# Performance work log

Hardware: AMD Instinct MI355X
Metric: run time of the kernel (lower is better)

Reference implementation:

```python
import jax, jax.numpy as jnp
import numpy as np

B, S, D, E, K = 4, 4096, 2048, 64, 8

def setup_inputs() -> dict:
    key = jax.random.key(0)
    k1, k2 = jax.random.split(key, 2)
    x = jax.random.normal(k1, (B, S, D), dtype=jnp.float32)
    # centroid projection params (Dense(features=n_experts))
    W = jax.random.normal(k2, (D, E), dtype=jnp.float32) / np.sqrt(D).astype(np.float32)
    b = jnp.zeros((E,), dtype=jnp.float32)
    return {"x": x, "W": W, "b": b, "k": K}

def reference(x, W, b, k):
    # dense gating projection + sigmoid -> per-token expert scores [B,S,E]
    scores = jax.nn.sigmoid(jnp.einsum('bsd,de->bse', x, W) + b)
    # per-token top-k expert selection (vectorized form of apply_along_axis(top))
    g_i, idx = jax.lax.top_k(scores, k)          # [B,S,k]
    g = g_i / jnp.sum(g_i, axis=-1, keepdims=True)  # renormalize top-k gates
    return g, idx, scores
```

## Files before the change

kernel.cpp:

```cpp
#include <hip/hip_runtime.h>
#include <math.h>
#include <stdint.h>

#define NTOK   16384
#define DDIM   2048
#define NE     64
#define TOPK   8

#define THREADS 512
#define TOKPB   16
#define BK      64
#define NCHUNK  (DDIM / BK)

#define XSLOTS   (TOKPB * (BK / 4))
#define WSLOTS   (BK * (NE / 4))
#define BUFSLOTS (XSLOTS + WSLOTS)
#define SMEMF4   (2 * BUFSLOTS)

__device__ __forceinline__ void gl_lds16(const void* g, void* l) {
    __builtin_amdgcn_global_load_lds(
        (const __attribute__((address_space(1))) void*)(uintptr_t)g,
        (__attribute__((address_space(3))) void*)(uintptr_t)l,
        16, 0, 0);
}

__global__ __launch_bounds__(THREADS, 6) void gate_kernel(
    const float* __restrict__ x, const float* __restrict__ W,
    const float* __restrict__ b, float* __restrict__ out)
{
    __shared__ float4 smem[SMEMF4];

    const int tid  = threadIdx.x;
    const int wave = tid >> 6;
    const int lane = tid & 63;
    const int ks   = tid >> 5;
    const int tg   = (tid >> 4) & 1;
    const int eg   = tid & 15;
    const int tok0 = blockIdx.x * TOKPB;

    const float* gx  = x + (size_t)(tok0 + wave * 4 + (lane >> 4)) * DDIM
                         + (lane & 15) * 4;
    const float* gw0 = W + (size_t)(wave * 8 + (lane >> 4)) * NE + (lane & 15) * 4;
    const float* gw1 = gw0 + (size_t)4 * NE;

    auto stage = [&](int c) {
        float4* Bf = &smem[(c & 1) * BUFSLOTS];
        const int kc = c * BK;
        if (wave < 4) gl_lds16(gx + kc, &Bf[wave * 64]);
        gl_lds16(gw0 + (size_t)kc * NE, &Bf[XSLOTS + wave * 128]);
        gl_lds16(gw1 + (size_t)kc * NE, &Bf[XSLOTS + wave * 128 + 64]);
    };

    float acc[8][4];
#pragma unroll
    for (int i = 0; i < 8; ++i)
#pragma unroll
        for (int m = 0; m < 4; ++m) acc[i][m] = 0.f;

    auto compute = [&](int c) {
        const float4* BX = &smem[(c & 1) * BUFSLOTS];
        const float4* BW = BX + XSLOTS;
        float4 wreg[4];
#pragma unroll
        for (int kk = 0; kk < 4; ++kk)
            wreg[kk] = BW[(ks * 4 + kk) * 16 + eg];
#pragma unroll
        for (int i = 0; i < 8; ++i) {
            const float4 xv = BX[(tg * 8 + i) * 16 + ks];
            const float* xp = (const float*)&xv;
#pragma unroll
            for (int kk = 0; kk < 4; ++kk) {
                const float xs = xp[kk];
                const float* wp = (const float*)&wreg[kk];
#pragma unroll
                for (int m = 0; m < 4; ++m)
                    acc[i][m] = fmaf(xs, wp[m], acc[i][m]);
            }
        }
    };

    stage(0);
#pragma unroll 1
    for (int c = 0; c < NCHUNK; ++c) {
        __syncthreads();
        if (c + 1 < NCHUNK) stage(c + 1);
        __builtin_amdgcn_s_setprio(1);
        compute(c);
        __builtin_amdgcn_s_setprio(0);
    }
    __syncthreads();

#pragma unroll
    for (int i = 0; i < 8; ++i)
#pragma unroll
        for (int m = 0; m < 4; ++m)
            acc[i][m] += __shfl_xor(acc[i][m], 32);

    float4* part4 = (float4*)smem;
    const int p = lane & 31;
    if (lane < 32) {
        float4* dst = part4 + (wave * 32 + p) * 9;
#pragma unroll
        for (int i = 0; i < 8; ++i)
            dst[i] = make_float4(acc[i][0], acc[i][1], acc[i][2], acc[i][3]);
    }
    __syncthreads();

    float* out_g   = out;
    float* out_idx = out + (size_t)NTOK * TOPK;
    float* out_s   = out + (size_t)NTOK * TOPK * 2;

    const int t  = tid >> 4;
    const int e4 = tid & 15;
    float4 sg = make_float4(0.f, 0.f, 0.f, 0.f);
    if (tid < 256) {
        const int cp = ((t >> 3) << 4) + e4;
        const int cf = t & 7;
        float sx = 0.f, sy = 0.f, sz = 0.f, sw = 0.f;
#pragma unroll
        for (int w = 0; w < 8; ++w) {
            const float4 v = part4[(w * 32 + cp) * 9 + cf];
            sx += v.x; sy += v.y; sz += v.z; sw += v.w;
        }
        const float4 bv = *(const float4*)(b + e4 * 4);
        sg.x = 1.f / (1.f + expf(-(sx + bv.x)));
        sg.y = 1.f / (1.f + expf(-(sy + bv.y)));
        sg.z = 1.f / (1.f + expf(-(sz + bv.z)));
        sg.w = 1.f / (1.f + expf(-(sw + bv.w)));
    }
    __syncthreads();

    float4* sc4 = (float4*)smem;
    if (tid < 256) {
        *(float4*)(out_s + (size_t)(tok0 + t) * NE + e4 * 4) = sg;
        sc4[t * 17 + e4] = sg;
    }
    __syncthreads();

    if (tid < 128) {
        const int tt = tid >> 3, lg = tid & 7;
        const float4 a0 = sc4[tt * 17 + lg * 2];
        const float4 a1 = sc4[tt * 17 + lg * 2 + 1];
        float s[8] = {a0.x, a0.y, a0.z, a0.w, a1.x, a1.y, a1.z, a1.w};
        float vsel = 0.f; int esel = 0; float ssum = 0.f;
#pragma unroll
        for (int j = 0; j < TOPK; ++j) {
            float bvv = s[0]; int be = 0;
#pragma unroll
            for (int m = 1; m < 8; ++m)
                if (s[m] > bvv) { bvv = s[m]; be = m; }
            float v = bvv; int ec = lg * 8 + be;
#pragma unroll
            for (int d = 1; d < 8; d <<= 1) {
                const float ov = __shfl_xor(v, d);
                const int   oe = __shfl_xor(ec, d);
                if (ov > v || (ov == v && oe < ec)) { v = ov; ec = oe; }
            }
            ssum += v;
            if (lg == j) { vsel = v; esel = ec; }
            if ((ec >> 3) == lg) {
                const int sl = ec & 7;
#pragma unroll
                for (int m = 0; m < 8; ++m)
                    if (sl == m) s[m] = -1.f;
            }
        }
        const float inv = 1.f / ssum;
        out_g  [(size_t)(tok0 + tt) * TOPK + lg] = vsel * inv;
        out_idx[(size_t)(tok0 + tt) * TOPK + lg] = (float)esel;
    }
}

extern "C" void kernel_launch(void* const* d_in, const int* in_sizes, int n_in,
                              void* d_out, int out_size, void* d_ws, size_t ws_size,
                              hipStream_t stream) {
    const float* x = (const float*)d_in[0];
    const float* W = (const float*)d_in[1];
    const float* b = (const float*)d_in[2];
    float* out = (float*)d_out;
    gate_kernel<<<NTOK / TOKPB, THREADS, 0, stream>>>(x, W, b, out);
}
```

Measured before the change: 248.4 us.

## Load W directly to registers and halve block size with 8x8 register tiles

The block size drops from 512 to 256 threads, and each thread now computes an 8-token by 8-expert register tile instead of 8x4. W is no longer staged through LDS. Each thread reads its 4x8 slice of W straight from global memory (expected to hit in cache) before issuing the async x stage, so only x is double-buffered in LDS. This cuts LDS traffic and footprint and doubles the FMAs per LDS read. The cost is a global-latency load of W inside every iteration, an extra cross-lane shuffle reduction step, and more registers per thread.

```diff
diff --git a/kernel.cpp b/kernel.cpp
--- a/kernel.cpp
+++ b/kernel.cpp
@@ -7,15 +7,12 @@
 #define NE     64
 #define TOPK   8
 
-#define THREADS 512
+#define THREADS 256
 #define TOKPB   16
 #define BK      64
 #define NCHUNK  (DDIM / BK)
 
-#define XSLOTS   (TOKPB * (BK / 4))
-#define WSLOTS   (BK * (NE / 4))
-#define BUFSLOTS (XSLOTS + WSLOTS)
-#define SMEMF4   (2 * BUFSLOTS)
+#define XSLOTS 256
 
 __device__ __forceinline__ void gl_lds16(const void* g, void* l) {
     __builtin_amdgcn_global_load_lds(
@@ -24,46 +21,50 @@
         16, 0, 0);
 }
 
-__global__ __launch_bounds__(THREADS, 6) void gate_kernel(
+__global__ __launch_bounds__(THREADS, 4) void gate_kernel(
     const float* __restrict__ x, const float* __restrict__ W,
     const float* __restrict__ b, float* __restrict__ out)
 {
-    __shared__ float4 smem[SMEMF4];
+    __shared__ float4 smem[1088];
 
     const int tid  = threadIdx.x;
     const int wave = tid >> 6;
     const int lane = tid & 63;
-    const int ks   = tid >> 5;
-    const int tg   = (tid >> 4) & 1;
-    const int eg   = tid & 15;
+    const int ks   = tid >> 4;
+    const int tg   = (tid >> 3) & 1;
+    const int eg   = tid & 7;
     const int tok0 = blockIdx.x * TOKPB;
 
-    const float* gx  = x + (size_t)(tok0 + wave * 4 + (lane >> 4)) * DDIM
-                         + (lane & 15) * 4;
-    const float* gw0 = W + (size_t)(wave * 8 + (lane >> 4)) * NE + (lane & 15) * 4;
-    const float* gw1 = gw0 + (size_t)4 * NE;
+    const float* gx = x + (size_t)(tok0 + wave * 4 + (lane >> 4)) * DDIM
+                        + (lane & 15) * 4;
+    const float* gw = W + (size_t)(ks * 4) * NE + eg * 8;
 
     auto stage = [&](int c) {
-        float4* Bf = &smem[(c & 1) * BUFSLOTS];
-        const int kc = c * BK;
-        if (wave < 4) gl_lds16(gx + kc, &Bf[wave * 64]);
-        gl_lds16(gw0 + (size_t)kc * NE, &Bf[XSLOTS + wave * 128]);
-        gl_lds16(gw1 + (size_t)kc * NE, &Bf[XSLOTS + wave * 128 + 64]);
+        gl_lds16(gx + c * BK, &smem[(c & 1) * XSLOTS + wave * 64]);
     };
 
-    float acc[8][4];
+    float acc[8][8];
 #pragma unroll
     for (int i = 0; i < 8; ++i)
 #pragma unroll
-        for (int m = 0; m < 4; ++m) acc[i][m] = 0.f;
+        for (int j = 0; j < 8; ++j) acc[i][j] = 0.f;
 
-    auto compute = [&](int c) {
-        const float4* BX = &smem[(c & 1) * BUFSLOTS];
-        const float4* BW = BX + XSLOTS;
-        float4 wreg[4];
+    stage(0);
+#pragma unroll 1
+    for (int c = 0; c < NCHUNK; ++c) {
+        __syncthreads();
+
+        const float* wb = gw + (size_t)(c * BK) * NE;
+        float4 wv[4][2];
 #pragma unroll
-        for (int kk = 0; kk < 4; ++kk)
-            wreg[kk] = BW[(ks * 4 + kk) * 16 + eg];
+        for (int kk = 0; kk < 4; ++kk) {
+            wv[kk][0] = *(const float4*)(wb + kk * NE);
+            wv[kk][1] = *(const float4*)(wb + kk * NE + 4);
+        }
+        __builtin_amdgcn_sched_barrier(0);
+        if (c + 1 < NCHUNK) stage(c + 1);
+
+        const float4* BX = &smem[(c & 1) * XSLOTS];
 #pragma unroll
         for (int i = 0; i < 8; ++i) {
             const float4 xv = BX[(tg * 8 + i) * 16 + ks];
@@ -71,38 +72,34 @@
 #pragma unroll
             for (int kk = 0; kk < 4; ++kk) {
                 const float xs = xp[kk];
-                const float* wp = (const float*)&wreg[kk];
+                const float* w0 = (const float*)&wv[kk][0];
+                const float* w1 = (const float*)&wv[kk][1];
 #pragma unroll
-                for (int m = 0; m < 4; ++m)
-                    acc[i][m] = fmaf(xs, wp[m], acc[i][m]);
+                for (int m = 0; m < 4; ++m) {
+                    acc[i][m]     = fmaf(xs, w0[m], acc[i][m]);
+                    acc[i][4 + m] = fmaf(xs, w1[m], acc[i][4 + m]);
+                }
             }
         }
-    };
-
-    stage(0);
-#pragma unroll 1
-    for (int c = 0; c < NCHUNK; ++c) {
-        __syncthreads();
-        if (c + 1 < NCHUNK) stage(c + 1);
-        __builtin_amdgcn_s_setprio(1);
-        compute(c);
-        __builtin_amdgcn_s_setprio(0);
     }
     __syncthreads();
 
 #pragma unroll
     for (int i = 0; i < 8; ++i)
 #pragma unroll
-        for (int m = 0; m < 4; ++m)
-            acc[i][m] += __shfl_xor(acc[i][m], 32);
+        for (int j = 0; j < 8; ++j) {
+            acc[i][j] += __shfl_xor(acc[i][j], 16);
+            acc[i][j] += __shfl_xor(acc[i][j], 32);
+        }
 
-    float4* part4 = (float4*)smem;
-    const int p = lane & 31;
-    if (lane < 32) {
-        float4* dst = part4 + (wave * 32 + p) * 9;
+    float4* part4 = smem;
+    if (lane < 16) {
+        float4* dst = part4 + (wave * 16 + lane) * 17;
 #pragma unroll
-        for (int i = 0; i < 8; ++i)
-            dst[i] = make_float4(acc[i][0], acc[i][1], acc[i][2], acc[i][3]);
+        for (int i = 0; i < 8; ++i) {
+            dst[i * 2]     = make_float4(acc[i][0], acc[i][1], acc[i][2], acc[i][3]);
+            dst[i * 2 + 1] = make_float4(acc[i][4], acc[i][5], acc[i][6], acc[i][7]);
+        }
     }
     __syncthreads();
 
@@ -110,31 +107,27 @@
     float* out_idx = out + (size_t)NTOK * TOPK;
     float* out_s   = out + (size_t)NTOK * TOPK * 2;
 
-    const int t  = tid >> 4;
-    const int e4 = tid & 15;
-    float4 sg = make_float4(0.f, 0.f, 0.f, 0.f);
-    if (tid < 256) {
-        const int cp = ((t >> 3) << 4) + e4;
-        const int cf = t & 7;
-        float sx = 0.f, sy = 0.f, sz = 0.f, sw = 0.f;
+    const int t   = tid >> 4;
+    const int e4  = tid & 15;
+    const int tg2 = t >> 3, i2 = t & 7;
+    const int eg2 = e4 >> 1, h2 = e4 & 1;
+    float4 sum = make_float4(0.f, 0.f, 0.f, 0.f);
 #pragma unroll
-        for (int w = 0; w < 8; ++w) {
-            const float4 v = part4[(w * 32 + cp) * 9 + cf];
-            sx += v.x; sy += v.y; sz += v.z; sw += v.w;
-        }
-        const float4 bv = *(const float4*)(b + e4 * 4);
-        sg.x = 1.f / (1.f + expf(-(sx + bv.x)));
-        sg.y = 1.f / (1.f + expf(-(sy + bv.y)));
-        sg.z = 1.f / (1.f + expf(-(sz + bv.z)));
-        sg.w = 1.f / (1.f + expf(-(sw + bv.w)));
+    for (int w = 0; w < 4; ++w) {
+        const float4 v = part4[(w * 16 + tg2 * 8 + eg2) * 17 + i2 * 2 + h2];
+        sum.x += v.x; sum.y += v.y; sum.z += v.z; sum.w += v.w;
     }
+    const float4 bv = *(const float4*)(b + e4 * 4);
+    float4 sg;
+    sg.x = 1.f / (1.f + expf(-(sum.x + bv.x)));
+    sg.y = 1.f / (1.f + expf(-(sum.y + bv.y)));
+    sg.z = 1.f / (1.f + expf(-(sum.z + bv.z)));
+    sg.w = 1.f / (1.f + expf(-(sum.w + bv.w)));
     __syncthreads();
 
-    float4* sc4 = (float4*)smem;
-    if (tid < 256) {
-        *(float4*)(out_s + (size_t)(tok0 + t) * NE + e4 * 4) = sg;
-        sc4[t * 17 + e4] = sg;
-    }
+    float4* sc4 = smem;
+    sc4[t * 17 + e4] = sg;
+    *(float4*)(out_s + (size_t)(tok0 + t) * NE + e4 * 4) = sg;
     __syncthreads();
 
     if (tid < 128) {
```

Result: faster. 234.5 us (-5.6%).
